# Kernel optimization log

Hardware: AMD Instinct MI355X
Metric: run time of the kernel (lower is better)

The kernel has to match this reference:

```python
import jax, jax.numpy as jnp
import numpy as np

EPS = 1e-10
BETA_SCALE = 1.0
TEMP = 0.5


def setup_inputs() -> dict:
    key = jax.random.key(0)
    ks = jax.random.split(key, 8)
    D = 128
    return {
        "root_mu_min": jax.random.normal(ks[0], (1, 64, D), dtype=jnp.float32),
        "root_mu_max": jax.random.normal(ks[1], (1, 64, D), dtype=jnp.float32),
        "root_beta_min_raw": jax.random.normal(ks[2], (1, 64, D), dtype=jnp.float32),
        "root_beta_max_raw": jax.random.normal(ks[3], (1, 64, D), dtype=jnp.float32),
        "adj_logits0": jax.random.normal(ks[4], (512, 64), dtype=jnp.float32),
        "adj_logits1": jax.random.normal(ks[5], (2048, 512), dtype=jnp.float32),
        "u0": jax.random.uniform(ks[6], (1, 512, 64), dtype=jnp.float32),
        "u1": jax.random.uniform(ks[7], (1, 2048, 512), dtype=jnp.float32),
    }


def _gumbel_sigmoid_hard(logits, u):
    # gumbel noise from externally supplied uniforms, straight-through hard threshold
    g = -jnp.log(-jnp.log(u + EPS) + EPS)
    y_soft = jax.nn.sigmoid((logits + g) / TEMP)
    y_hard = (y_soft > 0.5).astype(y_soft.dtype)
    return y_hard - jax.lax.stop_gradient(y_soft) + y_soft


def _weighted_intersection(mu_min, mu_max, beta_min, beta_max, w):
    # w: (1, C, P); parent boxes: (1, P, D)
    wsum = jnp.sum(w, axis=2)[..., None] + EPS                      # (1, C, 1)
    b_min = jnp.einsum('bcp,bpd->bcd', w, beta_min) / wsum           # (1, C, D)
    b_max = jnp.einsum('bcp,bpd->bcd', w, beta_max) / wsum           # (1, C, D)
    logw = jnp.log(w + EPS)[..., None]                               # (1, C, P, 1)
    arg_min = logw + mu_min[:, None, :, :] / b_min[:, :, None, :]    # (1, C, P, D)
    mu_min_i = b_min * jax.nn.logsumexp(arg_min, axis=2)             # (1, C, D)
    arg_max = logw - mu_max[:, None, :, :] / b_max[:, :, None, :]    # (1, C, P, D)
    mu_max_i = -b_max * jax.nn.logsumexp(arg_max, axis=2)            # (1, C, D)
    return mu_min_i, mu_max_i, b_min, b_max


def reference(root_mu_min, root_mu_max, root_beta_min_raw, root_beta_max_raw,
              adj_logits0, adj_logits1, u0, u1):
    beta_min = jax.nn.sigmoid(root_beta_min_raw) * BETA_SCALE + 1e-6
    beta_max = jax.nn.sigmoid(root_beta_max_raw) * BETA_SCALE + 1e-6
    level = (root_mu_min, root_mu_max, beta_min, beta_max)
    outs = list(level)
    for logits, u in ((adj_logits0, u0), (adj_logits1, u1)):
        w = _gumbel_sigmoid_hard(logits[None], u)  # (1, C, P)
        level = _weighted_intersection(*level, w)
        outs.extend(level)
    return tuple(outs)
```

## Files before the change

kernel.cpp:

```cpp
#include <hip/hip_runtime.h>
#include <cmath>

#define DD 128
#define LOG2E 1.4426950408889634f

__device__ __forceinline__ float sigm(float x) { return 1.0f / (1.0f + __expf(-x)); }

__device__ __forceinline__ unsigned fenc(float f) {
    unsigned b = __float_as_uint(f);
    return (b & 0x80000000u) ? ~b : (b | 0x80000000u);
}
__device__ __forceinline__ float fdec(unsigned e) {
    return (e & 0x80000000u) ? __uint_as_float(e ^ 0x80000000u) : __uint_as_float(~e);
}

__global__ __launch_bounds__(512)
void k_root0(const float* __restrict__ mu_min, const float* __restrict__ mu_max,
             const float* __restrict__ braw_min, const float* __restrict__ braw_max,
             float* __restrict__ out,
             float2* __restrict__ mu2_0, float2* __restrict__ bb2_0,
             unsigned* __restrict__ e_min0, unsigned* __restrict__ e_neg0) {
    __shared__ float r1[4][DD], r2[4][DD];
    const int i = blockIdx.x * 512 + threadIdx.x;
    const int rg = threadIdx.x >> 7, d = threadIdx.x & (DD - 1);
    float mn = mu_min[i], mx = mu_max[i];
    float bm = sigm(braw_min[i]) + 1e-6f;
    float bx = sigm(braw_max[i]) + 1e-6f;
    out[i] = mn; out[8192 + i] = mx; out[16384 + i] = bm; out[24576 + i] = bx;
    mu2_0[i] = make_float2(mn, mx);
    bb2_0[i] = make_float2(bm, bx);
    r1[rg][d] = mn; r2[rg][d] = -mx;
    __syncthreads();
    if (threadIdx.x < DD) {
        float a = fmaxf(fmaxf(r1[0][d], r1[1][d]), fmaxf(r1[2][d], r1[3][d]));
        float b = fmaxf(fmaxf(r2[0][d], r2[1][d]), fmaxf(r2[2][d], r2[3][d]));
        atomicMax(e_min0 + d, fenc(a));
        atomicMax(e_neg0 + d, fenc(b));
        if (blockIdx.x == 0) {
            mu2_0[64 * DD + d] = make_float2(-1e38f, 1e38f);
            bb2_0[64 * DD + d] = make_float2(0.0f, 0.0f);
        }
    }
}

template<int P, int RPB>
__global__ __launch_bounds__(512)
void k_packprep(const float* __restrict__ mu_min, const float* __restrict__ mu_max,
                const float* __restrict__ b_min, const float* __restrict__ b_max,
                float2* __restrict__ mu2, float2* __restrict__ bb2,
                unsigned* __restrict__ e_min, unsigned* __restrict__ e_neg) {
    __shared__ float s1[4][DD], s2[4][DD];
    const int d = threadIdx.x & (DD - 1);
    const int rg = threadIdx.x >> 7;
    const int r0 = blockIdx.x * RPB;
    float m1 = -INFINITY, m2 = -INFINITY;
    for (int r = rg; r < RPB; r += 4) {
        int i = (r0 + r) * DD + d;
        float a = mu_min[i], b = mu_max[i];
        mu2[i] = make_float2(a, b);
        bb2[i] = make_float2(b_min[i], b_max[i]);
        m1 = fmaxf(m1, a);
        m2 = fmaxf(m2, -b);
    }
    s1[rg][d] = m1; s2[rg][d] = m2;
    __syncthreads();
    if (threadIdx.x < DD) {
        float a = fmaxf(fmaxf(s1[0][d], s1[1][d]), fmaxf(s1[2][d], s1[3][d]));
        float b = fmaxf(fmaxf(s2[0][d], s2[1][d]), fmaxf(s2[2][d], s2[3][d]));
        atomicMax(e_min + d, fenc(a));
        atomicMax(e_neg + d, fenc(b));
        if (blockIdx.x == 0) {
            mu2[P * DD + d] = make_float2(-1e38f, 1e38f);
            bb2[P * DD + d] = make_float2(0.0f, 0.0f);
        }
    }
}

template<int P>
__global__ __launch_bounds__(256, 4)
void k_levelw(const float* __restrict__ logits, const float* __restrict__ u,
              const float2* __restrict__ bb2, const float2* __restrict__ mu2,
              const unsigned* __restrict__ e_min, const unsigned* __restrict__ e_neg,
              float* __restrict__ o_mu_min, float* __restrict__ o_mu_max,
              float* __restrict__ o_b_min, float* __restrict__ o_b_max) {
    __shared__ __align__(16) int plist[2][P];
    __shared__ float4 red[2][2][64];
    const int tid = threadIdx.x;
    const int w = tid >> 6;
    const int lane = tid & 63;
    const int j = w >> 1, h = w & 1;
    const int c = blockIdx.x * 2 + j;
    int* pl = plist[j];

    int base = 0;
    #pragma unroll
    for (int it = 0; it < P / 64; ++it) {
        int p = it * 64 + lane;
        int idx = c * P + p;
        float uu = u[idx] + 1e-10f;
        float g = -__logf(-__logf(uu) + 1e-10f);
        bool pres = (logits[idx] + g) > 0.0f;
        unsigned long long m = __ballot(pres);
        if (pres) {
            int pos = __popcll(m & ((1ull << lane) - 1));
            pl[base + pos] = p << 10;
        }
        base += (int)__popcll(m);
    }
    const int n = base;
    int npad = (n + 15) & ~15;
    if (npad == 0) npad = 16;
    if (lane < npad - n) pl[n + lane] = P << 10;

    const unsigned lb = (unsigned)(lane << 4);
    const char* bbc = (const char*)bb2;
    const char* muc = (const char*)mu2;
    const int Th = npad >> 4;

    float dmn0 = 0.f, dmx0 = 0.f, dmn1 = 0.f, dmx1 = 0.f;
    for (int t = 0; t < Th; ++t) {
        int k = h * 8 + t * 16;
        int4 A = *(const int4*)(pl + k);
        int4 B = *(const int4*)(pl + k + 4);
        float4 q0 = *(const float4*)(bbc + ((unsigned)A.x + lb));
        float4 q1 = *(const float4*)(bbc + ((unsigned)A.y + lb));
        float4 q2 = *(const float4*)(bbc + ((unsigned)A.z + lb));
        float4 q3 = *(const float4*)(bbc + ((unsigned)A.w + lb));
        float4 q4 = *(const float4*)(bbc + ((unsigned)B.x + lb));
        float4 q5 = *(const float4*)(bbc + ((unsigned)B.y + lb));
        float4 q6 = *(const float4*)(bbc + ((unsigned)B.z + lb));
        float4 q7 = *(const float4*)(bbc + ((unsigned)B.w + lb));
        dmn0 += (q0.x + q1.x) + (q2.x + q3.x) + (q4.x + q5.x) + (q6.x + q7.x);
        dmx0 += (q0.y + q1.y) + (q2.y + q3.y) + (q4.y + q5.y) + (q6.y + q7.y);
        dmn1 += (q0.z + q1.z) + (q2.z + q3.z) + (q4.z + q5.z) + (q6.z + q7.z);
        dmx1 += (q0.w + q1.w) + (q2.w + q3.w) + (q4.w + q5.w) + (q6.w + q7.w);
    }
    red[j][h][lane] = make_float4(dmn0, dmx0, dmn1, dmx1);
    __syncthreads();

    float4 pb0 = red[j][0][lane];
    float4 pb1 = red[j][1][lane];
    const float wsv = (float)n + 1e-10f;
    const float bmin0 = (pb0.x + pb1.x) / wsv;
    const float bmax0 = (pb0.y + pb1.y) / wsv;
    const float bmin1 = (pb0.z + pb1.z) / wsv;
    const float bmax1 = (pb0.w + pb1.w) / wsv;
    const float rmin0 = 1.0f / fmaxf(bmin0, 1e-30f);
    const float rmin1 = 1.0f / fmaxf(bmin1, 1e-30f);
    const float nrmax0 = -1.0f / fmaxf(bmax0, 1e-30f);
    const float nrmax1 = -1.0f / fmaxf(bmax1, 1e-30f);
    uint2 em = *(const uint2*)(e_min + 2 * lane);
    uint2 en = *(const uint2*)(e_neg + 2 * lane);
    const float Mm0 = fdec(em.x), Mm1 = fdec(em.y);
    const float Mg0 = fdec(en.x), Mg1 = fdec(en.y);
    const float rm20 = rmin0 * LOG2E, rm21 = rmin1 * LOG2E;
    const float nx20 = nrmax0 * LOG2E, nx21 = nrmax1 * LOG2E;
    const float nM10 = -rm20 * Mm0, nM11 = -rm21 * Mm1;
    const float nM20 = nx20 * Mg0, nM21 = nx21 * Mg1;
    __syncthreads();

    float s10 = 0.f, s20 = 0.f, s11 = 0.f, s21 = 0.f;
    for (int t = 0; t < Th; ++t) {
        int k = h * 8 + t * 16;
        int4 A = *(const int4*)(pl + k);
        int4 B = *(const int4*)(pl + k + 4);
        float4 q0 = *(const float4*)(muc + ((unsigned)A.x + lb));
        float4 q1 = *(const float4*)(muc + ((unsigned)A.y + lb));
        float4 q2 = *(const float4*)(muc + ((unsigned)A.z + lb));
        float4 q3 = *(const float4*)(muc + ((unsigned)A.w + lb));
        float4 q4 = *(const float4*)(muc + ((unsigned)B.x + lb));
        float4 q5 = *(const float4*)(muc + ((unsigned)B.y + lb));
        float4 q6 = *(const float4*)(muc + ((unsigned)B.z + lb));
        float4 q7 = *(const float4*)(muc + ((unsigned)B.w + lb));
        s10 += __builtin_amdgcn_exp2f(fmaf(q0.x, rm20, nM10));
        s20 += __builtin_amdgcn_exp2f(fmaf(q0.y, nx20, nM20));
        s11 += __builtin_amdgcn_exp2f(fmaf(q0.z, rm21, nM11));
        s21 += __builtin_amdgcn_exp2f(fmaf(q0.w, nx21, nM21));
        s10 += __builtin_amdgcn_exp2f(fmaf(q1.x, rm20, nM10));
        s20 += __builtin_amdgcn_exp2f(fmaf(q1.y, nx20, nM20));
        s11 += __builtin_amdgcn_exp2f(fmaf(q1.z, rm21, nM11));
        s21 += __builtin_amdgcn_exp2f(fmaf(q1.w, nx21, nM21));
        s10 += __builtin_amdgcn_exp2f(fmaf(q2.x, rm20, nM10));
        s20 += __builtin_amdgcn_exp2f(fmaf(q2.y, nx20, nM20));
        s11 += __builtin_amdgcn_exp2f(fmaf(q2.z, rm21, nM11));
        s21 += __builtin_amdgcn_exp2f(fmaf(q2.w, nx21, nM21));
        s10 += __builtin_amdgcn_exp2f(fmaf(q3.x, rm20, nM10));
        s20 += __builtin_amdgcn_exp2f(fmaf(q3.y, nx20, nM20));
        s11 += __builtin_amdgcn_exp2f(fmaf(q3.z, rm21, nM11));
        s21 += __builtin_amdgcn_exp2f(fmaf(q3.w, nx21, nM21));
        s10 += __builtin_amdgcn_exp2f(fmaf(q4.x, rm20, nM10));
        s20 += __builtin_amdgcn_exp2f(fmaf(q4.y, nx20, nM20));
        s11 += __builtin_amdgcn_exp2f(fmaf(q4.z, rm21, nM11));
        s21 += __builtin_amdgcn_exp2f(fmaf(q4.w, nx21, nM21));
        s10 += __builtin_amdgcn_exp2f(fmaf(q5.x, rm20, nM10));
        s20 += __builtin_amdgcn_exp2f(fmaf(q5.y, nx20, nM20));
        s11 += __builtin_amdgcn_exp2f(fmaf(q5.z, rm21, nM11));
        s21 += __builtin_amdgcn_exp2f(fmaf(q5.w, nx21, nM21));
        s10 += __builtin_amdgcn_exp2f(fmaf(q6.x, rm20, nM10));
        s20 += __builtin_amdgcn_exp2f(fmaf(q6.y, nx20, nM20));
        s11 += __builtin_amdgcn_exp2f(fmaf(q6.z, rm21, nM11));
        s21 += __builtin_amdgcn_exp2f(fmaf(q6.w, nx21, nM21));
        s10 += __builtin_amdgcn_exp2f(fmaf(q7.x, rm20, nM10));
        s20 += __builtin_amdgcn_exp2f(fmaf(q7.y, nx20, nM20));
        s11 += __builtin_amdgcn_exp2f(fmaf(q7.z, rm21, nM11));
        s21 += __builtin_amdgcn_exp2f(fmaf(q7.w, nx21, nM21));
    }
    red[j][h][lane] = make_float4(s10, s20, s11, s21);
    __syncthreads();

    if (h == 0) {
        float4 pc0 = red[j][0][lane];
        float4 pc1 = red[j][1][lane];
        const float S10 = fmaxf(pc0.x + pc1.x, 1e-35f);
        const float S20 = fmaxf(pc0.y + pc1.y, 1e-35f);
        const float S11 = fmaxf(pc0.z + pc1.z, 1e-35f);
        const float S21 = fmaxf(pc0.w + pc1.w, 1e-35f);
        const int idx = c * DD + 2 * lane;
        float v10 = bmin0 * fmaf(rmin0, Mm0, __logf(S10));
        float v11 = bmin1 * fmaf(rmin1, Mm1, __logf(S11));
        float v20 = -bmax0 * fmaf(-nrmax0, Mg0, __logf(S20));
        float v21 = -bmax1 * fmaf(-nrmax1, Mg1, __logf(S21));
        *(float2*)(o_mu_min + idx) = make_float2(v10, v11);
        *(float2*)(o_mu_max + idx) = make_float2(v20, v21);
        *(float2*)(o_b_min + idx)  = make_float2(bmin0, bmin1);
        *(float2*)(o_b_max + idx)  = make_float2(bmax0, bmax1);
    }
}

__global__ __launch_bounds__(512, 4)
void k_level2d(const float* __restrict__ logits, const float* __restrict__ u,
               const float2* __restrict__ bb2, const float2* __restrict__ mu2,
               const unsigned* __restrict__ e_min, const unsigned* __restrict__ e_neg,
               float* __restrict__ o_mu_min, float* __restrict__ o_mu_max,
               float* __restrict__ o_b_min, float* __restrict__ o_b_max) {
    constexpr int P = 512, TC = 4;
    __shared__ __align__(16) float wsh[P][TC];
    __shared__ int npres[TC];
    __shared__ float4 red[8][TC][64];
    __shared__ float4 carrA[TC][64], carrB[TC][64];
    const int tid = threadIdx.x;
    const int w = tid >> 6;
    const int lane = tid & 63;
    const int c0 = blockIdx.x * TC;
    if (tid < TC) npres[tid] = 0;
    __syncthreads();

    #pragma unroll
    for (int it = 0; it < TC; ++it) {
        int i = it * 512 + tid;
        int j = i >> 9;
        int p = i & 511;
        int idx = (c0 + j) * P + p;
        float uu = u[idx] + 1e-10f;
        float g = -__logf(-__logf(uu) + 1e-10f);
        bool pres = (logits[idx] + g) > 0.0f;
        wsh[p][j] = pres ? 1.0f : 1e-10f;
        unsigned long long m = __ballot(pres);
        if (lane == 0) atomicAdd(&npres[j], (int)__popcll(m));
    }
    __syncthreads();

    const unsigned lb = (unsigned)(lane << 4);
    const char* bbc = (const char*)bb2 + (unsigned)(w * 64) * 1024u + lb;
    const char* muc = (const char*)mu2 + (unsigned)(w * 64) * 1024u + lb;
    const int p0 = w * 64;

    float4 accB[TC];
    #pragma unroll
    for (int j = 0; j < TC; ++j) accB[j] = make_float4(0.f, 0.f, 0.f, 0.f);
    for (int z = 0; z < 64; z += 4) {
        float4 q0 = *(const float4*)(bbc + (unsigned)(z + 0) * 1024u);
        float4 q1 = *(const float4*)(bbc + (unsigned)(z + 1) * 1024u);
        float4 q2 = *(const float4*)(bbc + (unsigned)(z + 2) * 1024u);
        float4 q3 = *(const float4*)(bbc + (unsigned)(z + 3) * 1024u);
        float4 w0 = *(const float4*)wsh[p0 + z + 0];
        float4 w1 = *(const float4*)wsh[p0 + z + 1];
        float4 w2 = *(const float4*)wsh[p0 + z + 2];
        float4 w3 = *(const float4*)wsh[p0 + z + 3];
        const float* wf0 = (const float*)&w0;
        const float* wf1 = (const float*)&w1;
        const float* wf2 = (const float*)&w2;
        const float* wf3 = (const float*)&w3;
        #pragma unroll
        for (int j = 0; j < TC; ++j) {
            accB[j].x = fmaf(wf0[j], q0.x, fmaf(wf1[j], q1.x, fmaf(wf2[j], q2.x, fmaf(wf3[j], q3.x, accB[j].x))));
            accB[j].y = fmaf(wf0[j], q0.y, fmaf(wf1[j], q1.y, fmaf(wf2[j], q2.y, fmaf(wf3[j], q3.y, accB[j].y))));
            accB[j].z = fmaf(wf0[j], q0.z, fmaf(wf1[j], q1.z, fmaf(wf2[j], q2.z, fmaf(wf3[j], q3.z, accB[j].z))));
            accB[j].w = fmaf(wf0[j], q0.w, fmaf(wf1[j], q1.w, fmaf(wf2[j], q2.w, fmaf(wf3[j], q3.w, accB[j].w))));
        }
    }
    #pragma unroll
    for (int j = 0; j < TC; ++j) red[w][j][lane] = accB[j];
    __syncthreads();

    float bmin0, bmax0, bmin1, bmax1, rmin0, rmin1, nrmax0, nrmax1, Mm0, Mm1, Mg0, Mg1;
    const int rj = tid >> 6;
    if (tid < 256) {
        float4 S = red[0][rj][lane];
        #pragma unroll
        for (int ww = 1; ww < 8; ++ww) {
            float4 t = red[ww][rj][lane];
            S.x += t.x; S.y += t.y; S.z += t.z; S.w += t.w;
        }
        const float wsv = (float)npres[rj] + 1e-10f;
        bmin0 = S.x / wsv; bmax0 = S.y / wsv; bmin1 = S.z / wsv; bmax1 = S.w / wsv;
        rmin0 = 1.0f / fmaxf(bmin0, 1e-30f);
        rmin1 = 1.0f / fmaxf(bmin1, 1e-30f);
        nrmax0 = -1.0f / fmaxf(bmax0, 1e-30f);
        nrmax1 = -1.0f / fmaxf(bmax1, 1e-30f);
        uint2 em = *(const uint2*)(e_min + 2 * lane);
        uint2 en = *(const uint2*)(e_neg + 2 * lane);
        Mm0 = fdec(em.x); Mm1 = fdec(em.y);
        Mg0 = fdec(en.x); Mg1 = fdec(en.y);
        float rm20 = rmin0 * LOG2E, rm21 = rmin1 * LOG2E;
        float nx20 = nrmax0 * LOG2E, nx21 = nrmax1 * LOG2E;
        carrA[rj][lane] = make_float4(rm20, rm21, nx20, nx21);
        carrB[rj][lane] = make_float4(-rm20 * Mm0, -rm21 * Mm1, nx20 * Mg0, nx21 * Mg1);
    }
    __syncthreads();

    float4 cA[TC], cB[TC];
    #pragma unroll
    for (int j = 0; j < TC; ++j) { cA[j] = carrA[j][lane]; cB[j] = carrB[j][lane]; }

    float4 accS[TC];
    #pragma unroll
    for (int j = 0; j < TC; ++j) accS[j] = make_float4(0.f, 0.f, 0.f, 0.f);
    for (int z = 0; z < 64; z += 2) {
        float4 q0 = *(const float4*)(muc + (unsigned)(z + 0) * 1024u);
        float4 q1 = *(const float4*)(muc + (unsigned)(z + 1) * 1024u);
        float4 w0 = *(const float4*)wsh[p0 + z + 0];
        float4 w1 = *(const float4*)wsh[p0 + z + 1];
        const float* wf0 = (const float*)&w0;
        const float* wf1 = (const float*)&w1;
        #pragma unroll
        for (int j = 0; j < TC; ++j) {
            accS[j].x = fmaf(wf0[j], __builtin_amdgcn_exp2f(fmaf(q0.x, cA[j].x, cB[j].x)), accS[j].x);
            accS[j].y = fmaf(wf0[j], __builtin_amdgcn_exp2f(fmaf(q0.y, cA[j].z, cB[j].z)), accS[j].y);
            accS[j].z = fmaf(wf0[j], __builtin_amdgcn_exp2f(fmaf(q0.z, cA[j].y, cB[j].y)), accS[j].z);
            accS[j].w = fmaf(wf0[j], __builtin_amdgcn_exp2f(fmaf(q0.w, cA[j].w, cB[j].w)), accS[j].w);
            accS[j].x = fmaf(wf1[j], __builtin_amdgcn_exp2f(fmaf(q1.x, cA[j].x, cB[j].x)), accS[j].x);
            accS[j].y = fmaf(wf1[j], __builtin_amdgcn_exp2f(fmaf(q1.y, cA[j].z, cB[j].z)), accS[j].y);
            accS[j].z = fmaf(wf1[j], __builtin_amdgcn_exp2f(fmaf(q1.z, cA[j].y, cB[j].y)), accS[j].z);
            accS[j].w = fmaf(wf1[j], __builtin_amdgcn_exp2f(fmaf(q1.w, cA[j].w, cB[j].w)), accS[j].w);
        }
    }
    #pragma unroll
    for (int j = 0; j < TC; ++j) red[w][j][lane] = accS[j];
    __syncthreads();

    if (tid < 256) {
        float4 S = red[0][rj][lane];
        #pragma unroll
        for (int ww = 1; ww < 8; ++ww) {
            float4 t = red[ww][rj][lane];
            S.x += t.x; S.y += t.y; S.z += t.z; S.w += t.w;
        }
        const float S10 = fmaxf(S.x, 1e-35f);
        const float S20 = fmaxf(S.y, 1e-35f);
        const float S11 = fmaxf(S.z, 1e-35f);
        const float S21 = fmaxf(S.w, 1e-35f);
        const int idx = (c0 + rj) * DD + 2 * lane;
        float v10 = bmin0 * fmaf(rmin0, Mm0, __logf(S10));
        float v11 = bmin1 * fmaf(rmin1, Mm1, __logf(S11));
        float v20 = -bmax0 * fmaf(-nrmax0, Mg0, __logf(S20));
        float v21 = -bmax1 * fmaf(-nrmax1, Mg1, __logf(S21));
        *(float2*)(o_mu_min + idx) = make_float2(v10, v11);
        *(float2*)(o_mu_max + idx) = make_float2(v20, v21);
        *(float2*)(o_b_min + idx)  = make_float2(bmin0, bmin1);
        *(float2*)(o_b_max + idx)  = make_float2(bmax0, bmax1);
    }
}

extern "C" void kernel_launch(void* const* d_in, const int* in_sizes, int n_in,
                              void* d_out, int out_size, void* d_ws, size_t ws_size,
                              hipStream_t stream) {
    const float* mu_min0  = (const float*)d_in[0];
    const float* mu_max0  = (const float*)d_in[1];
    const float* braw_min = (const float*)d_in[2];
    const float* braw_max = (const float*)d_in[3];
    const float* adj0     = (const float*)d_in[4];
    const float* adj1     = (const float*)d_in[5];
    const float* u0       = (const float*)d_in[6];
    const float* u1       = (const float*)d_in[7];
    float* out = (float*)d_out;
    float* ws = (float*)d_ws;

    unsigned* cm_enc  = (unsigned*)ws;
    unsigned* cm0_min = cm_enc;
    unsigned* cm0_neg = cm_enc + 128;
    unsigned* cm1_min = cm_enc + 256;
    unsigned* cm1_neg = cm_enc + 384;
    float2* mu2_0 = (float2*)(ws + 512);
    float2* bb2_0 = mu2_0 + 65 * DD;
    float2* mu2_1 = bb2_0 + 65 * DD;
    float2* bb2_1 = mu2_1 + 513 * DD;


    hipMemsetAsync(cm_enc, 0, 512 * sizeof(unsigned), stream);

    k_root0<<<dim3(16), dim3(512), 0, stream>>>(
        mu_min0, mu_max0, braw_min, braw_max, out, mu2_0, bb2_0, cm0_min, cm0_neg);

    k_levelw<64><<<dim3(256), dim3(256), 0, stream>>>(
        adj0, u0, bb2_0, mu2_0, cm0_min, cm0_neg,
        out + 32768, out + 98304, out + 163840, out + 229376);

    k_packprep<512, 8><<<dim3(64), dim3(512), 0, stream>>>(
        out + 32768, out + 98304, out + 163840, out + 229376, mu2_1, bb2_1, cm1_min, cm1_neg);

    k_level2d<<<dim3(512), dim3(512), 0, stream>>>(
        adj1, u1, bb2_1, mu2_1, cm1_min, cm1_neg,
        out + 294912, out + 557056, out + 819200, out + 1081344);
}
```

Measured before the change: 125.4 us.

## Fuse root prep, level-1 intersection and level-2 packing into one kernel

Replaces the three kernels for root sigmoid/packing, level-1 weighted intersection and level-2 pack/prep with a single kernel, k_lvl1. Each block recomputes the 64 parent rows and their per-dimension maxima locally instead of reading global atomics, then handles 4 children with dense weighted sums. It writes the packed level-2 inputs and the column maxima directly. This removes two kernel launches and their global round-trips, at the cost of redundant root recomputation in every block and a dense pass over all parents instead of only the present ones. The level-2 kernel's weight-sampling index arithmetic is also simplified.

New measurement: 137.0 us. 9.2% more time.

```diff
diff --git a/kernel.cpp b/kernel.cpp
--- a/kernel.cpp
+++ b/kernel.cpp
@@ -14,216 +14,166 @@
     return (e & 0x80000000u) ? __uint_as_float(e ^ 0x80000000u) : __uint_as_float(~e);
 }
 
-__global__ __launch_bounds__(512)
-void k_root0(const float* __restrict__ mu_min, const float* __restrict__ mu_max,
-             const float* __restrict__ braw_min, const float* __restrict__ braw_max,
-             float* __restrict__ out,
-             float2* __restrict__ mu2_0, float2* __restrict__ bb2_0,
-             unsigned* __restrict__ e_min0, unsigned* __restrict__ e_neg0) {
-    __shared__ float r1[4][DD], r2[4][DD];
-    const int i = blockIdx.x * 512 + threadIdx.x;
-    const int rg = threadIdx.x >> 7, d = threadIdx.x & (DD - 1);
-    float mn = mu_min[i], mx = mu_max[i];
-    float bm = sigm(braw_min[i]) + 1e-6f;
-    float bx = sigm(braw_max[i]) + 1e-6f;
-    out[i] = mn; out[8192 + i] = mx; out[16384 + i] = bm; out[24576 + i] = bx;
-    mu2_0[i] = make_float2(mn, mx);
-    bb2_0[i] = make_float2(bm, bx);
-    r1[rg][d] = mn; r2[rg][d] = -mx;
-    __syncthreads();
-    if (threadIdx.x < DD) {
-        float a = fmaxf(fmaxf(r1[0][d], r1[1][d]), fmaxf(r1[2][d], r1[3][d]));
-        float b = fmaxf(fmaxf(r2[0][d], r2[1][d]), fmaxf(r2[2][d], r2[3][d]));
-        atomicMax(e_min0 + d, fenc(a));
-        atomicMax(e_neg0 + d, fenc(b));
-        if (blockIdx.x == 0) {
-            mu2_0[64 * DD + d] = make_float2(-1e38f, 1e38f);
-            bb2_0[64 * DD + d] = make_float2(0.0f, 0.0f);
-        }
-    }
-}
-
-template<int P, int RPB>
-__global__ __launch_bounds__(512)
-void k_packprep(const float* __restrict__ mu_min, const float* __restrict__ mu_max,
-                const float* __restrict__ b_min, const float* __restrict__ b_max,
-                float2* __restrict__ mu2, float2* __restrict__ bb2,
-                unsigned* __restrict__ e_min, unsigned* __restrict__ e_neg) {
-    __shared__ float s1[4][DD], s2[4][DD];
-    const int d = threadIdx.x & (DD - 1);
-    const int rg = threadIdx.x >> 7;
-    const int r0 = blockIdx.x * RPB;
-    float m1 = -INFINITY, m2 = -INFINITY;
-    for (int r = rg; r < RPB; r += 4) {
-        int i = (r0 + r) * DD + d;
-        float a = mu_min[i], b = mu_max[i];
-        mu2[i] = make_float2(a, b);
-        bb2[i] = make_float2(b_min[i], b_max[i]);
-        m1 = fmaxf(m1, a);
-        m2 = fmaxf(m2, -b);
-    }
-    s1[rg][d] = m1; s2[rg][d] = m2;
-    __syncthreads();
-    if (threadIdx.x < DD) {
-        float a = fmaxf(fmaxf(s1[0][d], s1[1][d]), fmaxf(s1[2][d], s1[3][d]));
-        float b = fmaxf(fmaxf(s2[0][d], s2[1][d]), fmaxf(s2[2][d], s2[3][d]));
-        atomicMax(e_min + d, fenc(a));
-        atomicMax(e_neg + d, fenc(b));
-        if (blockIdx.x == 0) {
-            mu2[P * DD + d] = make_float2(-1e38f, 1e38f);
-            bb2[P * DD + d] = make_float2(0.0f, 0.0f);
-        }
-    }
-}
-
-template<int P>
-__global__ __launch_bounds__(256, 4)
-void k_levelw(const float* __restrict__ logits, const float* __restrict__ u,
-              const float2* __restrict__ bb2, const float2* __restrict__ mu2,
-              const unsigned* __restrict__ e_min, const unsigned* __restrict__ e_neg,
-              float* __restrict__ o_mu_min, float* __restrict__ o_mu_max,
-              float* __restrict__ o_b_min, float* __restrict__ o_b_max) {
-    __shared__ __align__(16) int plist[2][P];
-    __shared__ float4 red[2][2][64];
+__global__ __launch_bounds__(512, 4)
+void k_lvl1(const float* __restrict__ mu_min0, const float* __restrict__ mu_max0,
+            const float* __restrict__ braw_min, const float* __restrict__ braw_max,
+            const float* __restrict__ adj0, const float* __restrict__ u0,
+            float* __restrict__ out,
+            float2* __restrict__ mu2_1, float2* __restrict__ bb2_1,
+            unsigned* __restrict__ cm1_min, unsigned* __restrict__ cm1_neg) {
+    __shared__ __align__(16) float wsh[64][4];
+    __shared__ int npres[4];
+    __shared__ float4 red[8][4][64];
+    __shared__ float4 cmx[8][64];
+    __shared__ float4 carrA[4][64], carrB[4][64];
     const int tid = threadIdx.x;
-    const int w = tid >> 6;
-    const int lane = tid & 63;
-    const int j = w >> 1, h = w & 1;
-    const int c = blockIdx.x * 2 + j;
-    int* pl = plist[j];
-
-    int base = 0;
-    #pragma unroll
-    for (int it = 0; it < P / 64; ++it) {
-        int p = it * 64 + lane;
-        int idx = c * P + p;
-        float uu = u[idx] + 1e-10f;
+    const int w = tid >> 6, lane = tid & 63;
+    const int c0 = blockIdx.x * 4;
+
+    if (tid < 64) {
+        int i = blockIdx.x * 64 + tid;
+        out[i] = mu_min0[i];
+        out[8192 + i] = mu_max0[i];
+        out[16384 + i] = sigm(braw_min[i]) + 1e-6f;
+        out[24576 + i] = sigm(braw_max[i]) + 1e-6f;
+    }
+
+    if (tid < 256) {
+        int j = tid >> 6, p = tid & 63;
+        int idx = (c0 + j) * 64 + p;
+        float uu = u0[idx] + 1e-10f;
         float g = -__logf(-__logf(uu) + 1e-10f);
-        bool pres = (logits[idx] + g) > 0.0f;
+        bool pres = (adj0[idx] + g) > 0.0f;
+        wsh[p][j] = pres ? 1.0f : 1e-10f;
         unsigned long long m = __ballot(pres);
-        if (pres) {
-            int pos = __popcll(m & ((1ull << lane) - 1));
-            pl[base + pos] = p << 10;
-        }
-        base += (int)__popcll(m);
-    }
-    const int n = base;
-    int npad = (n + 15) & ~15;
-    if (npad == 0) npad = 16;
-    if (lane < npad - n) pl[n + lane] = P << 10;
-
-    const unsigned lb = (unsigned)(lane << 4);
-    const char* bbc = (const char*)bb2;
-    const char* muc = (const char*)mu2;
-    const int Th = npad >> 4;
-
-    float dmn0 = 0.f, dmx0 = 0.f, dmn1 = 0.f, dmx1 = 0.f;
-    for (int t = 0; t < Th; ++t) {
-        int k = h * 8 + t * 16;
-        int4 A = *(const int4*)(pl + k);
-        int4 B = *(const int4*)(pl + k + 4);
-        float4 q0 = *(const float4*)(bbc + ((unsigned)A.x + lb));
-        float4 q1 = *(const float4*)(bbc + ((unsigned)A.y + lb));
-        float4 q2 = *(const float4*)(bbc + ((unsigned)A.z + lb));
-        float4 q3 = *(const float4*)(bbc + ((unsigned)A.w + lb));
-        float4 q4 = *(const float4*)(bbc + ((unsigned)B.x + lb));
-        float4 q5 = *(const float4*)(bbc + ((unsigned)B.y + lb));
-        float4 q6 = *(const float4*)(bbc + ((unsigned)B.z + lb));
-        float4 q7 = *(const float4*)(bbc + ((unsigned)B.w + lb));
-        dmn0 += (q0.x + q1.x) + (q2.x + q3.x) + (q4.x + q5.x) + (q6.x + q7.x);
-        dmx0 += (q0.y + q1.y) + (q2.y + q3.y) + (q4.y + q5.y) + (q6.y + q7.y);
-        dmn1 += (q0.z + q1.z) + (q2.z + q3.z) + (q4.z + q5.z) + (q6.z + q7.z);
-        dmx1 += (q0.w + q1.w) + (q2.w + q3.w) + (q4.w + q5.w) + (q6.w + q7.w);
-    }
-    red[j][h][lane] = make_float4(dmn0, dmx0, dmn1, dmx1);
-    __syncthreads();
-
-    float4 pb0 = red[j][0][lane];
-    float4 pb1 = red[j][1][lane];
-    const float wsv = (float)n + 1e-10f;
-    const float bmin0 = (pb0.x + pb1.x) / wsv;
-    const float bmax0 = (pb0.y + pb1.y) / wsv;
-    const float bmin1 = (pb0.z + pb1.z) / wsv;
-    const float bmax1 = (pb0.w + pb1.w) / wsv;
-    const float rmin0 = 1.0f / fmaxf(bmin0, 1e-30f);
-    const float rmin1 = 1.0f / fmaxf(bmin1, 1e-30f);
-    const float nrmax0 = -1.0f / fmaxf(bmax0, 1e-30f);
-    const float nrmax1 = -1.0f / fmaxf(bmax1, 1e-30f);
-    uint2 em = *(const uint2*)(e_min + 2 * lane);
-    uint2 en = *(const uint2*)(e_neg + 2 * lane);
-    const float Mm0 = fdec(em.x), Mm1 = fdec(em.y);
-    const float Mg0 = fdec(en.x), Mg1 = fdec(en.y);
-    const float rm20 = rmin0 * LOG2E, rm21 = rmin1 * LOG2E;
-    const float nx20 = nrmax0 * LOG2E, nx21 = nrmax1 * LOG2E;
-    const float nM10 = -rm20 * Mm0, nM11 = -rm21 * Mm1;
-    const float nM20 = nx20 * Mg0, nM21 = nx21 * Mg1;
-    __syncthreads();
-
-    float s10 = 0.f, s20 = 0.f, s11 = 0.f, s21 = 0.f;
-    for (int t = 0; t < Th; ++t) {
-        int k = h * 8 + t * 16;
-        int4 A = *(const int4*)(pl + k);
-        int4 B = *(const int4*)(pl + k + 4);
-        float4 q0 = *(const float4*)(muc + ((unsigned)A.x + lb));
-        float4 q1 = *(const float4*)(muc + ((unsigned)A.y + lb));
-        float4 q2 = *(const float4*)(muc + ((unsigned)A.z + lb));
-        float4 q3 = *(const float4*)(muc + ((unsigned)A.w + lb));
-        float4 q4 = *(const float4*)(muc + ((unsigned)B.x + lb));
-        float4 q5 = *(const float4*)(muc + ((unsigned)B.y + lb));
-        float4 q6 = *(const float4*)(muc + ((unsigned)B.z + lb));
-        float4 q7 = *(const float4*)(muc + ((unsigned)B.w + lb));
-        s10 += __builtin_amdgcn_exp2f(fmaf(q0.x, rm20, nM10));
-        s20 += __builtin_amdgcn_exp2f(fmaf(q0.y, nx20, nM20));
-        s11 += __builtin_amdgcn_exp2f(fmaf(q0.z, rm21, nM11));
-        s21 += __builtin_amdgcn_exp2f(fmaf(q0.w, nx21, nM21));
-        s10 += __builtin_amdgcn_exp2f(fmaf(q1.x, rm20, nM10));
-        s20 += __builtin_amdgcn_exp2f(fmaf(q1.y, nx20, nM20));
-        s11 += __builtin_amdgcn_exp2f(fmaf(q1.z, rm21, nM11));
-        s21 += __builtin_amdgcn_exp2f(fmaf(q1.w, nx21, nM21));
-        s10 += __builtin_amdgcn_exp2f(fmaf(q2.x, rm20, nM10));
-        s20 += __builtin_amdgcn_exp2f(fmaf(q2.y, nx20, nM20));
-        s11 += __builtin_amdgcn_exp2f(fmaf(q2.z, rm21, nM11));
-        s21 += __builtin_amdgcn_exp2f(fmaf(q2.w, nx21, nM21));
-        s10 += __builtin_amdgcn_exp2f(fmaf(q3.x, rm20, nM10));
-        s20 += __builtin_amdgcn_exp2f(fmaf(q3.y, nx20, nM20));
-        s11 += __builtin_amdgcn_exp2f(fmaf(q3.z, rm21, nM11));
-        s21 += __builtin_amdgcn_exp2f(fmaf(q3.w, nx21, nM21));
-        s10 += __builtin_amdgcn_exp2f(fmaf(q4.x, rm20, nM10));
-        s20 += __builtin_amdgcn_exp2f(fmaf(q4.y, nx20, nM20));
-        s11 += __builtin_amdgcn_exp2f(fmaf(q4.z, rm21, nM11));
-        s21 += __builtin_amdgcn_exp2f(fmaf(q4.w, nx21, nM21));
-        s10 += __builtin_amdgcn_exp2f(fmaf(q5.x, rm20, nM10));
-        s20 += __builtin_amdgcn_exp2f(fmaf(q5.y, nx20, nM20));
-        s11 += __builtin_amdgcn_exp2f(fmaf(q5.z, rm21, nM11));
-        s21 += __builtin_amdgcn_exp2f(fmaf(q5.w, nx21, nM21));
-        s10 += __builtin_amdgcn_exp2f(fmaf(q6.x, rm20, nM10));
-        s20 += __builtin_amdgcn_exp2f(fmaf(q6.y, nx20, nM20));
-        s11 += __builtin_amdgcn_exp2f(fmaf(q6.z, rm21, nM11));
-        s21 += __builtin_amdgcn_exp2f(fmaf(q6.w, nx21, nM21));
-        s10 += __builtin_amdgcn_exp2f(fmaf(q7.x, rm20, nM10));
-        s20 += __builtin_amdgcn_exp2f(fmaf(q7.y, nx20, nM20));
-        s11 += __builtin_amdgcn_exp2f(fmaf(q7.z, rm21, nM11));
-        s21 += __builtin_amdgcn_exp2f(fmaf(q7.w, nx21, nM21));
-    }
-    red[j][h][lane] = make_float4(s10, s20, s11, s21);
-    __syncthreads();
-
-    if (h == 0) {
-        float4 pc0 = red[j][0][lane];
-        float4 pc1 = red[j][1][lane];
-        const float S10 = fmaxf(pc0.x + pc1.x, 1e-35f);
-        const float S20 = fmaxf(pc0.y + pc1.y, 1e-35f);
-        const float S11 = fmaxf(pc0.z + pc1.z, 1e-35f);
-        const float S21 = fmaxf(pc0.w + pc1.w, 1e-35f);
-        const int idx = c * DD + 2 * lane;
+        if ((tid & 63) == 0) npres[j] = (int)__popcll(m);
+    }
+    __syncthreads();
+
+    const int p0 = w * 8;
+    const int dbase = 2 * lane;
+
+    float4 accB[4];
+    #pragma unroll
+    for (int j = 0; j < 4; ++j) accB[j] = make_float4(0.f, 0.f, 0.f, 0.f);
+    float4 mrow[8];
+    float cm_mn0 = -INFINITY, cm_mn1 = -INFINITY, cm_ng0 = -INFINITY, cm_ng1 = -INFINITY;
+    #pragma unroll
+    for (int z = 0; z < 8; ++z) {
+        int p = p0 + z;
+        float2 bmr = *(const float2*)(braw_min + p * DD + dbase);
+        float2 bxr = *(const float2*)(braw_max + p * DD + dbase);
+        float2 mnr = *(const float2*)(mu_min0 + p * DD + dbase);
+        float2 mxr = *(const float2*)(mu_max0 + p * DD + dbase);
+        float bm0 = sigm(bmr.x) + 1e-6f, bm1 = sigm(bmr.y) + 1e-6f;
+        float bx0 = sigm(bxr.x) + 1e-6f, bx1 = sigm(bxr.y) + 1e-6f;
+        mrow[z] = make_float4(mnr.x, mxr.x, mnr.y, mxr.y);
+        cm_mn0 = fmaxf(cm_mn0, mnr.x); cm_mn1 = fmaxf(cm_mn1, mnr.y);
+        cm_ng0 = fmaxf(cm_ng0, -mxr.x); cm_ng1 = fmaxf(cm_ng1, -mxr.y);
+        float4 wv = *(const float4*)wsh[p];
+        const float* wf = (const float*)&wv;
+        #pragma unroll
+        for (int j = 0; j < 4; ++j) {
+            accB[j].x = fmaf(wf[j], bm0, accB[j].x);
+            accB[j].y = fmaf(wf[j], bx0, accB[j].y);
+            accB[j].z = fmaf(wf[j], bm1, accB[j].z);
+            accB[j].w = fmaf(wf[j], bx1, accB[j].w);
+        }
+    }
+    #pragma unroll
+    for (int j = 0; j < 4; ++j) red[w][j][lane] = accB[j];
+    cmx[w][lane] = make_float4(cm_mn0, cm_ng0, cm_mn1, cm_ng1);
+    __syncthreads();
+
+    float bmin0, bmax0, bmin1, bmax1, rmin0, rmin1, nrmax0, nrmax1, Mm0, Mm1, Mg0, Mg1;
+    const int rj = tid >> 6;
+    if (tid < 256) {
+        float4 S = red[0][rj][lane];
+        float4 M = cmx[0][lane];
+        #pragma unroll
+        for (int ww = 1; ww < 8; ++ww) {
+            float4 t = red[ww][rj][lane];
+            S.x += t.x; S.y += t.y; S.z += t.z; S.w += t.w;
+            float4 m = cmx[ww][lane];
+            M.x = fmaxf(M.x, m.x); M.y = fmaxf(M.y, m.y);
+            M.z = fmaxf(M.z, m.z); M.w = fmaxf(M.w, m.w);
+        }
+        Mm0 = M.x; Mg0 = M.y; Mm1 = M.z; Mg1 = M.w;
+        const float wsv = (float)npres[rj] + 1e-10f;
+        bmin0 = S.x / wsv; bmax0 = S.y / wsv; bmin1 = S.z / wsv; bmax1 = S.w / wsv;
+        rmin0 = 1.0f / fmaxf(bmin0, 1e-30f);
+        rmin1 = 1.0f / fmaxf(bmin1, 1e-30f);
+        nrmax0 = -1.0f / fmaxf(bmax0, 1e-30f);
+        nrmax1 = -1.0f / fmaxf(bmax1, 1e-30f);
+        float rm20 = rmin0 * LOG2E, rm21 = rmin1 * LOG2E;
+        float nx20 = nrmax0 * LOG2E, nx21 = nrmax1 * LOG2E;
+        carrA[rj][lane] = make_float4(rm20, rm21, nx20, nx21);
+        carrB[rj][lane] = make_float4(-rm20 * Mm0, -rm21 * Mm1, nx20 * Mg0, nx21 * Mg1);
+    }
+    __syncthreads();
+
+    float4 cA[4], cB[4];
+    #pragma unroll
+    for (int j = 0; j < 4; ++j) { cA[j] = carrA[j][lane]; cB[j] = carrB[j][lane]; }
+
+    float4 accS[4];
+    #pragma unroll
+    for (int j = 0; j < 4; ++j) accS[j] = make_float4(0.f, 0.f, 0.f, 0.f);
+    #pragma unroll
+    for (int z = 0; z < 8; ++z) {
+        float4 q = mrow[z];
+        float4 wv = *(const float4*)wsh[p0 + z];
+        const float* wf = (const float*)&wv;
+        #pragma unroll
+        for (int j = 0; j < 4; ++j) {
+            accS[j].x = fmaf(wf[j], __builtin_amdgcn_exp2f(fmaf(q.x, cA[j].x, cB[j].x)), accS[j].x);
+            accS[j].y = fmaf(wf[j], __builtin_amdgcn_exp2f(fmaf(q.y, cA[j].z, cB[j].z)), accS[j].y);
+            accS[j].z = fmaf(wf[j], __builtin_amdgcn_exp2f(fmaf(q.z, cA[j].y, cB[j].y)), accS[j].z);
+            accS[j].w = fmaf(wf[j], __builtin_amdgcn_exp2f(fmaf(q.w, cA[j].w, cB[j].w)), accS[j].w);
+        }
+    }
+    #pragma unroll
+    for (int j = 0; j < 4; ++j) red[w][j][lane] = accS[j];
+    __syncthreads();
+
+    if (tid < 256) {
+        float4 S = red[0][rj][lane];
+        #pragma unroll
+        for (int ww = 1; ww < 8; ++ww) {
+            float4 t = red[ww][rj][lane];
+            S.x += t.x; S.y += t.y; S.z += t.z; S.w += t.w;
+        }
+        const float S10 = fmaxf(S.x, 1e-35f);
+        const float S20 = fmaxf(S.y, 1e-35f);
+        const float S11 = fmaxf(S.z, 1e-35f);
+        const float S21 = fmaxf(S.w, 1e-35f);
+        const int cc = c0 + rj;
+        const int idx = cc * DD + 2 * lane;
         float v10 = bmin0 * fmaf(rmin0, Mm0, __logf(S10));
         float v11 = bmin1 * fmaf(rmin1, Mm1, __logf(S11));
         float v20 = -bmax0 * fmaf(-nrmax0, Mg0, __logf(S20));
         float v21 = -bmax1 * fmaf(-nrmax1, Mg1, __logf(S21));
-        *(float2*)(o_mu_min + idx) = make_float2(v10, v11);
-        *(float2*)(o_mu_max + idx) = make_float2(v20, v21);
-        *(float2*)(o_b_min + idx)  = make_float2(bmin0, bmin1);
-        *(float2*)(o_b_max + idx)  = make_float2(bmax0, bmax1);
+        *(float2*)(out + 32768 + idx)  = make_float2(v10, v11);
+        *(float2*)(out + 98304 + idx)  = make_float2(v20, v21);
+        *(float2*)(out + 163840 + idx) = make_float2(bmin0, bmin1);
+        *(float2*)(out + 229376 + idx) = make_float2(bmax0, bmax1);
+        *(float4*)(mu2_1 + idx) = make_float4(v10, v20, v11, v21);
+        *(float4*)(bb2_1 + idx) = make_float4(bmin0, bmax0, bmin1, bmax1);
+        red[0][rj][lane] = make_float4(v10, -v20, v11, -v21);
+    }
+    __syncthreads();
+    if (tid < 64) {
+        float4 m = red[0][0][tid];
+        #pragma unroll
+        for (int jj = 1; jj < 4; ++jj) {
+            float4 t = red[0][jj][tid];
+            m.x = fmaxf(m.x, t.x); m.y = fmaxf(m.y, t.y);
+            m.z = fmaxf(m.z, t.z); m.w = fmaxf(m.w, t.w);
+        }
+        atomicMax(cm1_min + 2 * tid,     fenc(m.x));
+        atomicMax(cm1_neg + 2 * tid,     fenc(m.y));
+        atomicMax(cm1_min + 2 * tid + 1, fenc(m.z));
+        atomicMax(cm1_neg + 2 * tid + 1, fenc(m.w));
     }
 }
 
@@ -247,16 +197,13 @@
 
     #pragma unroll
     for (int it = 0; it < TC; ++it) {
-        int i = it * 512 + tid;
-        int j = i >> 9;
-        int p = i & 511;
-        int idx = (c0 + j) * P + p;
+        int idx = (c0 + it) * P + tid;
         float uu = u[idx] + 1e-10f;
         float g = -__logf(-__logf(uu) + 1e-10f);
         bool pres = (logits[idx] + g) > 0.0f;
-        wsh[p][j] = pres ? 1.0f : 1e-10f;
+        wsh[tid][it] = pres ? 1.0f : 1e-10f;
         unsigned long long m = __ballot(pres);
-        if (lane == 0) atomicAdd(&npres[j], (int)__popcll(m));
+        if (lane == 0) atomicAdd(&npres[it], (int)__popcll(m));
     }
     __syncthreads();
 
@@ -387,27 +334,17 @@
     float* ws = (float*)d_ws;
 
     unsigned* cm_enc  = (unsigned*)ws;
-    unsigned* cm0_min = cm_enc;
-    unsigned* cm0_neg = cm_enc + 128;
     unsigned* cm1_min = cm_enc + 256;
     unsigned* cm1_neg = cm_enc + 384;
-    float2* mu2_0 = (float2*)(ws + 512);
-    float2* bb2_0 = mu2_0 + 65 * DD;
-    float2* mu2_1 = bb2_0 + 65 * DD;
+    float2* mu2_1 = (float2*)(ws + 512);
     float2* bb2_1 = mu2_1 + 513 * DD;
 
 
-    hipMemsetAsync(cm_enc, 0, 512 * sizeof(unsigned), stream);
-
-    k_root0<<<dim3(16), dim3(512), 0, stream>>>(
-        mu_min0, mu_max0, braw_min, braw_max, out, mu2_0, bb2_0, cm0_min, cm0_neg);
-
-    k_levelw<64><<<dim3(256), dim3(256), 0, stream>>>(
-        adj0, u0, bb2_0, mu2_0, cm0_min, cm0_neg,
-        out + 32768, out + 98304, out + 163840, out + 229376);
-
-    k_packprep<512, 8><<<dim3(64), dim3(512), 0, stream>>>(
-        out + 32768, out + 98304, out + 163840, out + 229376, mu2_1, bb2_1, cm1_min, cm1_neg);
+    hipMemsetAsync(cm_enc + 256, 0, 256 * sizeof(unsigned), stream);
+
+    k_lvl1<<<dim3(128), dim3(512), 0, stream>>>(
+        mu_min0, mu_max0, braw_min, braw_max, adj0, u0,
+        out, mu2_1, bb2_1, cm1_min, cm1_neg);
 
     k_level2d<<<dim3(512), dim3(512), 0, stream>>>(
         adj1, u1, bb2_1, mu2_1, cm1_min, cm1_neg,
```
